# Optimization experiments

Measured on AMD Instinct MI355X. Metric: run time of the kernel, lower is better.

The kernel has to match this reference:

```python
import jax, jax.numpy as jnp
import numpy as np

N_HEADS = 8
EMBED = 640
CROSS = 768
HEAD = EMBED // N_HEADS


def setup_inputs() -> dict:
    key = jax.random.key(0)
    ks = jax.random.split(key, 10)
    s_e = 1.0 / np.sqrt(EMBED)
    s_c = 1.0 / np.sqrt(CROSS)
    return {
        "x": jax.random.normal(ks[0], (8, 4096, EMBED), jnp.float32),
        "y": jax.random.normal(ks[1], (8, 77, CROSS), jnp.float32),
        "Wq": jax.random.uniform(ks[2], (EMBED, EMBED), jnp.float32, -s_e, s_e),
        "bq": jax.random.uniform(ks[3], (EMBED,), jnp.float32, -s_e, s_e),
        "Wk": jax.random.uniform(ks[4], (CROSS, EMBED), jnp.float32, -s_c, s_c),
        "bk": jax.random.uniform(ks[5], (EMBED,), jnp.float32, -s_c, s_c),
        "Wv": jax.random.uniform(ks[6], (CROSS, EMBED), jnp.float32, -s_c, s_c),
        "bv": jax.random.uniform(ks[7], (EMBED,), jnp.float32, -s_c, s_c),
        "Wo": jax.random.uniform(ks[8], (EMBED, EMBED), jnp.float32, -s_e, s_e),
        "bo": jax.random.uniform(ks[9], (EMBED,), jnp.float32, -s_e, s_e),
    }


def reference(x, y, Wq, bq, Wk, bk, Wv, bv, Wo, bo):
    B, T, C = x.shape
    S = y.shape[1]
    # projections; split heads: [B, H, T, D]
    q = (x @ Wq + bq).reshape(B, T, N_HEADS, HEAD).transpose(0, 2, 1, 3)
    k = (y @ Wk + bk).reshape(B, S, N_HEADS, HEAD).transpose(0, 2, 1, 3)
    v = (y @ Wv + bv).reshape(B, S, N_HEADS, HEAD).transpose(0, 2, 1, 3)
    scores = jnp.einsum("bhtd,bhsd->bhts", q, k) / jnp.sqrt(jnp.float32(HEAD))
    attn = jax.nn.softmax(scores, axis=-1)
    out = jnp.einsum("bhts,bhsd->bhtd", attn, v)
    out = out.transpose(0, 2, 1, 3).reshape(B, T, C)
    return out @ Wo + bo
```

## Files before the change

### kernel.cpp

```cpp
#include <hip/hip_runtime.h>
#include <hip/hip_bf16.h>
#include <hip/hip_fp16.h>

#define EMBED 640
#define CROSS 768
#define NH 8
#define HEAD 80
#define BATCH 8
#define SEQT 4096
#define SEQS 77
#define MROWS (BATCH * SEQT)

typedef _Float16 half8 __attribute__((ext_vector_type(8)));
typedef float floatx4 __attribute__((ext_vector_type(4)));

__device__ __forceinline__ void lds_load16(const void* g, void* l) {
    __builtin_amdgcn_global_load_lds(
        (const __attribute__((address_space(1))) void*)g,
        (__attribute__((address_space(3))) void*)l, 16, 0, 0);
}

__global__ __launch_bounds__(256) void cvt_f32_f16(
    const float* __restrict__ in, _Float16* __restrict__ out)
{
    size_t i = ((size_t)blockIdx.x * 256 + threadIdx.x) * 8;
    float4 a = *(const float4*)&in[i];
    float4 b = *(const float4*)&in[i + 4];
    half8 h;
    h[0] = (_Float16)a.x; h[1] = (_Float16)a.y;
    h[2] = (_Float16)a.z; h[3] = (_Float16)a.w;
    h[4] = (_Float16)b.x; h[5] = (_Float16)b.y;
    h[6] = (_Float16)b.z; h[7] = (_Float16)b.w;
    *(half8*)&out[i] = h;
}

__global__ __launch_bounds__(256) void transpose_all(
    const float* __restrict__ Wq, const float* __restrict__ Wo,
    const float* __restrict__ Wk, const float* __restrict__ Wv,
    _Float16* __restrict__ wqt, _Float16* __restrict__ wot,
    _Float16* __restrict__ wkt, _Float16* __restrict__ wvt)
{
    __shared__ float t[32][33];
    const int z = blockIdx.z;
    const float* W;  _Float16* Wt;  int K;
    if      (z == 0) { W = Wq; Wt = wqt; K = EMBED; }
    else if (z == 1) { W = Wo; Wt = wot; K = EMBED; }
    else if (z == 2) { W = Wk; Wt = wkt; K = CROSS; }
    else             { W = Wv; Wt = wvt; K = CROSS; }
    const int N = EMBED;
    const int k0 = blockIdx.y * 32, n0 = blockIdx.x * 32;
    if (k0 >= K) return;
    for (int r = threadIdx.y; r < 32; r += 8)
        t[r][threadIdx.x] = W[(size_t)(k0 + r) * N + n0 + threadIdx.x];
    __syncthreads();
    for (int r = threadIdx.y; r < 32; r += 8)
        Wt[(size_t)(n0 + r) * K + k0 + threadIdx.x] = (_Float16)t[threadIdx.x][r];
}

__global__ __launch_bounds__(256) void cvt_y_zero(
    const float* __restrict__ y, _Float16* __restrict__ yh,
    _Float16* __restrict__ vth)
{
    const size_t i = (size_t)blockIdx.x * 256 + threadIdx.x;
    if (i < (size_t)640 * CROSS / 8) {
        const size_t e = i * 8;
        half8 h = {};
        if (e < (size_t)BATCH * SEQS * CROSS) {
            float4 a = *(const float4*)&y[e];
            float4 b = *(const float4*)&y[e + 4];
            h[0] = (_Float16)a.x; h[1] = (_Float16)a.y;
            h[2] = (_Float16)a.z; h[3] = (_Float16)a.w;
            h[4] = (_Float16)b.x; h[5] = (_Float16)b.y;
            h[6] = (_Float16)b.z; h[7] = (_Float16)b.w;
        }
        *(half8*)&yh[e] = h;
    } else {
        const size_t j = (i - (size_t)640 * CROSS / 8) * 8;
        *(half8*)&vth[j] = (half8){};
    }
}

template <bool HALF_OUT>
__global__ __launch_bounds__(256) void gemm_f16(
    const _Float16* __restrict__ A,
    const _Float16* __restrict__ Bt,
    const float* __restrict__ bias,
    void* __restrict__ Cout, int M, int N, int K, float scale)
{
    __shared__ _Float16 As[2][128 * 64];
    __shared__ _Float16 Bs[2][128 * 64];

    const int tid  = threadIdx.x;
    const int wave = tid >> 6;
    const int lane = tid & 63;
    const int quad = lane >> 4;
    const int l16  = lane & 15;

    const int l   = blockIdx.y * gridDim.x + blockIdx.x;
    const int inner = l >> 3;
    const int p   = (l & 7) + 8 * (inner / gridDim.x);
    const int nt  = inner % gridDim.x;
    const int m0 = p * 128, n0 = nt * 128;
    const int wm = (wave >> 1) * 64, wn = (wave & 1) * 64;

    const int srow = wave * 32 + (lane >> 3);
    const int sch  = ((lane & 7) ^ (lane >> 3)) * 8;
    const _Float16* gA[4];
    const _Float16* gB[4];
    #pragma unroll
    for (int q = 0; q < 4; ++q) {
        gA[q] = &A [(size_t)(m0 + srow + q * 8) * K + sch];
        gB[q] = &Bt[(size_t)(n0 + srow + q * 8) * K + sch];
    }

    const int NT = K / 64;

    auto stage = [&](int t, int bf) {
        const size_t off = (size_t)t * 64;
        #pragma unroll
        for (int q = 0; q < 4; ++q) {
            lds_load16(gA[q] + off, &As[bf][(wave * 4 + q) * 512]);
            lds_load16(gB[q] + off, &Bs[bf][(wave * 4 + q) * 512]);
        }
    };
    stage(0, 0);

    floatx4 acc[4][4] = {};

    for (int t = 0; t < NT; ++t) {
        const int bf = t & 1;
        if (t + 1 < NT) {
            stage(t + 1, bf ^ 1);
            asm volatile("s_waitcnt vmcnt(8)" ::: "memory");
        } else {
            asm volatile("s_waitcnt vmcnt(0)" ::: "memory");
        }
        __builtin_amdgcn_s_barrier();
        __builtin_amdgcn_sched_barrier(0);

        const _Float16* as = As[bf];
        const _Float16* bs = Bs[bf];
        __builtin_amdgcn_s_setprio(1);
        #pragma unroll
        for (int k = 0; k < 2; ++k) {
            half8 a[4], b[4];
            #pragma unroll
            for (int i = 0; i < 4; ++i)
                a[i] = *(const half8*)&as[(wm + i * 16 + l16) * 64 +
                                          (((k * 4 + quad) ^ (l16 & 7)) * 8)];
            #pragma unroll
            for (int j = 0; j < 4; ++j)
                b[j] = *(const half8*)&bs[(wn + j * 16 + l16) * 64 +
                                          (((k * 4 + quad) ^ (l16 & 7)) * 8)];
            #pragma unroll
            for (int i = 0; i < 4; ++i)
                #pragma unroll
                for (int j = 0; j < 4; ++j)
                    acc[i][j] = __builtin_amdgcn_mfma_f32_16x16x32_f16(
                        a[i], b[j], acc[i][j], 0, 0, 0);
        }
        __builtin_amdgcn_s_setprio(0);

        asm volatile("s_waitcnt lgkmcnt(0)" ::: "memory");
        __builtin_amdgcn_sched_barrier(0);
        __builtin_amdgcn_s_barrier();
    }

    float bcol[4];
    #pragma unroll
    for (int j = 0; j < 4; ++j) bcol[j] = bias[n0 + wn + j * 16 + l16];
    #pragma unroll
    for (int i = 0; i < 4; ++i)
        #pragma unroll
        for (int r = 0; r < 4; ++r) {
            const int m = m0 + wm + i * 16 + quad * 4 + r;
            #pragma unroll
            for (int j = 0; j < 4; ++j) {
                float v = (acc[i][j][r] + bcol[j]) * scale;
                const size_t off = (size_t)m * N + n0 + wn + j * 16 + l16;
                if (HALF_OUT) ((_Float16*)Cout)[off] = (_Float16)v;
                else          ((float*)Cout)[off] = v;
            }
        }
}

__global__ __launch_bounds__(256) void kv_gemm(
    const _Float16* __restrict__ yh,
    const _Float16* __restrict__ Wkt, const _Float16* __restrict__ Wvt,
    const float* __restrict__ bk, const float* __restrict__ bv,
    _Float16* __restrict__ kh, _Float16* __restrict__ vth)
{
    __shared__ _Float16 As[64 * 32];
    __shared__ _Float16 Bs[64 * 32];

    const int tid = threadIdx.x;
    const int wave = tid >> 6, lane = tid & 63;
    const int quad = lane >> 4, l16 = lane & 15;
    const int m0 = blockIdx.y * 64, n0 = blockIdx.x * 64;
    const bool isV = blockIdx.z != 0;
    const _Float16* Bt = isV ? Wvt : Wkt;
    const float* bias  = isV ? bv : bk;

    const int row = tid >> 2;
    const int kch = (tid & 3) * 8;

    floatx4 acc[4] = {};

    for (int k0 = 0; k0 < CROSS; k0 += 32) {
        lds_load16(&yh[(size_t)(m0 + row) * CROSS + k0 + kch], &As[wave * 512]);
        lds_load16(&Bt[(size_t)(n0 + row) * CROSS + k0 + kch], &Bs[wave * 512]);
        __syncthreads();
        half8 b = *(const half8*)&Bs[(wave * 16 + l16) * 32 + quad * 8];
        #pragma unroll
        for (int i = 0; i < 4; ++i) {
            half8 a = *(const half8*)&As[(i * 16 + l16) * 32 + quad * 8];
            acc[i] = __builtin_amdgcn_mfma_f32_16x16x32_f16(a, b, acc[i], 0, 0, 0);
        }
        __syncthreads();
    }

    const int n = n0 + wave * 16 + l16;
    const int h = n / HEAD, d = n % HEAD;
    const float bb = bias[n];
    #pragma unroll
    for (int i = 0; i < 4; ++i)
        #pragma unroll
        for (int r = 0; r < 4; ++r) {
            const int m = m0 + i * 16 + quad * 4 + r;
            if (m >= BATCH * SEQS) continue;
            const int b_ = m / SEQS, s = m % SEQS;
            const int bh = b_ * NH + h;
            const float v = acc[i][r] + bb;
            if (isV) vth[(size_t)bh * (HEAD * 80) + d * 80 + s] = (_Float16)v;
            else     kh [(size_t)bh * (SEQS * HEAD) + s * HEAD + d] = (_Float16)v;
        }
}

__global__ __launch_bounds__(256, 4) void attn_mfma(
    const _Float16* __restrict__ qh,
    const _Float16* __restrict__ kh,
    const _Float16* __restrict__ vth,
    _Float16* __restrict__ oh)
{
    constexpr int LS = 88;
    __shared__ _Float16 lds[(80 + 80 + 64) * LS + 8];
    _Float16* Ks = lds;
    _Float16* Vt = lds + 80 * LS;
    _Float16* Ps = lds + 160 * LS;

    const int tid = threadIdx.x;
    const int wave = tid >> 6, lane = tid & 63;
    const int quad = lane >> 4, l16 = lane & 15;
    const int bh = blockIdx.y;
    const int b = bh >> 3, h = bh & 7;
    const size_t row0 = (size_t)b * SEQT + (size_t)blockIdx.x * 256;
    const half8 hz = {};

    const _Float16* qp = qh + (row0 + wave * 16 + l16) * EMBED + h * HEAD;

    half8 qa0 = *(const half8*)&qp[quad * 8];
    half8 qa1 = *(const half8*)&qp[32 + quad * 8];
    half8 qa2 = (quad < 2) ? *(const half8*)&qp[64 + quad * 8] : hz;

    for (int idx = tid; idx < 80 * 11; idx += 256) {
        const int s = idx / 11, c = idx % 11;
        half8 v = hz;
        if (s < SEQS && c < 10)
            v = *(const half8*)&kh[(size_t)bh * (SEQS * HEAD) + s * HEAD + c * 8];
        *(half8*)&Ks[s * LS + c * 8] = v;
    }
    for (int idx = tid; idx < 80 * 11; idx += 256) {
        const int d = idx / 11, c = idx % 11;
        half8 v = hz;
        if (c < 10)
            v = *(const half8*)&vth[(size_t)bh * (HEAD * 80) + d * 80 + c * 8];
        *(half8*)&Vt[d * LS + c * 8] = v;
    }
    __syncthreads();

    for (int t = 0; t < 4; ++t) {
        floatx4 accs[5] = {};
        #pragma unroll
        for (int st = 0; st < 5; ++st) {
            const _Float16* kr = &Ks[(st * 16 + l16) * LS];
            half8 b0 = *(const half8*)&kr[quad * 8];
            half8 b1 = *(const half8*)&kr[32 + quad * 8];
            half8 b2 = *(const half8*)&kr[64 + quad * 8];
            accs[st] = __builtin_amdgcn_mfma_f32_16x16x32_f16(qa0, b0, accs[st], 0, 0, 0);
            accs[st] = __builtin_amdgcn_mfma_f32_16x16x32_f16(qa1, b1, accs[st], 0, 0, 0);
            accs[st] = __builtin_amdgcn_mfma_f32_16x16x32_f16(qa2, b2, accs[st], 0, 0, 0);
        }
        if (l16 >= 13) {
            accs[4][0] = -1e30f; accs[4][1] = -1e30f;
            accs[4][2] = -1e30f; accs[4][3] = -1e30f;
        }

        float recip[4];
        #pragma unroll
        for (int r = 0; r < 4; ++r) {
            float m = accs[0][r];
            #pragma unroll
            for (int st = 1; st < 5; ++st) m = fmaxf(m, accs[st][r]);
            m = fmaxf(m, __shfl_xor(m, 1));
            m = fmaxf(m, __shfl_xor(m, 2));
            m = fmaxf(m, __shfl_xor(m, 4));
            m = fmaxf(m, __shfl_xor(m, 8));
            float l = 0.f;
            const int row = wave * 16 + quad * 4 + r;
            #pragma unroll
            for (int st = 0; st < 5; ++st) {
                float e = __expf(accs[st][r] - m);
                l += e;
                Ps[row * LS + st * 16 + l16] = (_Float16)e;
            }
            l += __shfl_xor(l, 1);
            l += __shfl_xor(l, 2);
            l += __shfl_xor(l, 4);
            l += __shfl_xor(l, 8);
            recip[r] = 1.0f / l;
        }
        __syncthreads();

        half8 qn0 = hz, qn1 = hz, qn2 = hz;
        if (t < 3) {
            const _Float16* qn = qp + (size_t)(t + 1) * 64 * EMBED;
            qn0 = *(const half8*)&qn[quad * 8];
            qn1 = *(const half8*)&qn[32 + quad * 8];
            if (quad < 2) qn2 = *(const half8*)&qn[64 + quad * 8];
        }

        const _Float16* pr = &Ps[(wave * 16 + l16) * LS];
        half8 pa0 = *(const half8*)&pr[quad * 8];
        half8 pa1 = *(const half8*)&pr[32 + quad * 8];
        half8 pa2 = (quad < 2) ? *(const half8*)&pr[64 + quad * 8] : hz;
        __syncthreads();

        floatx4 acco[5] = {};
        #pragma unroll
        for (int dt = 0; dt < 5; ++dt) {
            const _Float16* vr = &Vt[(dt * 16 + l16) * LS];
            half8 b0 = *(const half8*)&vr[quad * 8];
            half8 b1 = *(const half8*)&vr[32 + quad * 8];
            half8 b2 = *(const half8*)&vr[64 + quad * 8];
            acco[dt] = __builtin_amdgcn_mfma_f32_16x16x32_f16(pa0, b0, acco[dt], 0, 0, 0);
            acco[dt] = __builtin_amdgcn_mfma_f32_16x16x32_f16(pa1, b1, acco[dt], 0, 0, 0);
            acco[dt] = __builtin_amdgcn_mfma_f32_16x16x32_f16(pa2, b2, acco[dt], 0, 0, 0);
        }

        #pragma unroll
        for (int r = 0; r < 4; ++r) {
            const size_t grow = row0 + t * 64 + wave * 16 + quad * 4 + r;
            #pragma unroll
            for (int dt = 0; dt < 5; ++dt)
                oh[grow * EMBED + h * HEAD + dt * 16 + l16] =
                    (_Float16)(acco[dt][r] * recip[r]);
        }

        qa0 = qn0; qa1 = qn1; qa2 = qn2;
    }
}

extern "C" void kernel_launch(void* const* d_in, const int* in_sizes, int n_in,
                              void* d_out, int out_size, void* d_ws, size_t ws_size,
                              hipStream_t stream)
{
    const float* x  = (const float*)d_in[0];
    const float* y  = (const float*)d_in[1];
    const float* Wq = (const float*)d_in[2];
    const float* bq = (const float*)d_in[3];
    const float* Wk = (const float*)d_in[4];
    const float* bk = (const float*)d_in[5];
    const float* Wv = (const float*)d_in[6];
    const float* bv = (const float*)d_in[7];
    const float* Wo = (const float*)d_in[8];
    const float* bo = (const float*)d_in[9];
    float* out = (float*)d_out;

    const size_t ME = (size_t)MROWS * EMBED;
    _Float16* xh  = (_Float16*)d_ws;
    _Float16* qh  = xh + ME;
    _Float16* ah  = qh + ME;
    _Float16* kh  = ah + ME;
    _Float16* vth = kh  + (size_t)BATCH * NH * SEQS * HEAD;
    _Float16* wqt = vth + (size_t)BATCH * NH * HEAD * 80;
    _Float16* wot = wqt + (size_t)EMBED * EMBED;
    _Float16* yh  = wot + (size_t)EMBED * EMBED;
    _Float16* wkt = yh  + (size_t)640 * CROSS;
    _Float16* wvt = wkt + (size_t)EMBED * CROSS;

    transpose_all<<<dim3(EMBED / 32, CROSS / 32, 4), dim3(32, 8), 0, stream>>>(
        Wq, Wo, Wk, Wv, wqt, wot, wkt, wvt);
    cvt_y_zero<<<dim3(440), 256, 0, stream>>>(y, yh, vth);
    cvt_f32_f16<<<dim3(ME / (256 * 8)), 256, 0, stream>>>(x, xh);

    gemm_f16<true><<<dim3(EMBED / 128, MROWS / 128), 256, 0, stream>>>(
        xh, wqt, bq, qh, MROWS, EMBED, EMBED, 0.11180339887498949f);
    kv_gemm<<<dim3(EMBED / 64, 640 / 64, 2), 256, 0, stream>>>(
        yh, wkt, wvt, bk, bv, kh, vth);
    attn_mfma<<<dim3(SEQT / 256, BATCH * NH), 256, 0, stream>>>(qh, kh, vth, ah);
    gemm_f16<false><<<dim3(EMBED / 128, MROWS / 128), 256, 0, stream>>>(
        ah, wot, bo, out, MROWS, EMBED, EMBED, 1.0f);
}
```

Before: 288.2 us.

## Fuse fp32-to-fp16 conversion of x into the Q projection GEMM

Removes the standalone cvt_f32_f16 pass over x and adds a dedicated gemm_q kernel. It loads fp32 x tiles into registers, converts them to fp16 and writes them into swizzled LDS, while B tiles are staged with direct global-to-LDS loads in a double-buffered pipeline. This saves a full write and re-read of the fp16 copy of x (about 42 MB of traffic) and one kernel launch. In exchange the GEMM reads twice as many bytes for A, holds more registers for the prefetched fp32 data, and relies on hand-placed waitcnt counts being right.

```diff
diff --git a/kernel.cpp b/kernel.cpp
--- a/kernel.cpp
+++ b/kernel.cpp
@@ -18,20 +18,6 @@
     __builtin_amdgcn_global_load_lds(
         (const __attribute__((address_space(1))) void*)g,
         (__attribute__((address_space(3))) void*)l, 16, 0, 0);
-}
-
-__global__ __launch_bounds__(256) void cvt_f32_f16(
-    const float* __restrict__ in, _Float16* __restrict__ out)
-{
-    size_t i = ((size_t)blockIdx.x * 256 + threadIdx.x) * 8;
-    float4 a = *(const float4*)&in[i];
-    float4 b = *(const float4*)&in[i + 4];
-    half8 h;
-    h[0] = (_Float16)a.x; h[1] = (_Float16)a.y;
-    h[2] = (_Float16)a.z; h[3] = (_Float16)a.w;
-    h[4] = (_Float16)b.x; h[5] = (_Float16)b.y;
-    h[6] = (_Float16)b.z; h[7] = (_Float16)b.w;
-    *(half8*)&out[i] = h;
 }
 
 __global__ __launch_bounds__(256) void transpose_all(
@@ -184,6 +170,148 @@
         }
 }
 
+__global__ __launch_bounds__(256) void gemm_q(
+    const float* __restrict__ x,
+    const _Float16* __restrict__ Bt,
+    const float* __restrict__ bias,
+    _Float16* __restrict__ Cout)
+{
+    constexpr int K = EMBED, N = EMBED;
+    __shared__ _Float16 As[2][128 * 64];
+    __shared__ _Float16 Bs[2][128 * 64];
+
+    const int tid  = threadIdx.x;
+    const int wave = tid >> 6;
+    const int lane = tid & 63;
+    const int quad = lane >> 4;
+    const int l16  = lane & 15;
+
+    const int l   = blockIdx.y * gridDim.x + blockIdx.x;
+    const int inner = l >> 3;
+    const int p   = (l & 7) + 8 * (inner / gridDim.x);
+    const int nt  = inner % gridDim.x;
+    const int m0 = p * 128, n0 = nt * 128;
+    const int wm = (wave >> 1) * 64, wn = (wave & 1) * 64;
+
+    const int srow = wave * 32 + (lane >> 3);
+    const int sch  = ((lane & 7) ^ (lane >> 3)) * 8;
+    const _Float16* gB[4];
+    #pragma unroll
+    for (int q = 0; q < 4; ++q)
+        gB[q] = &Bt[(size_t)(n0 + srow + q * 8) * K + sch];
+
+    const int ar = tid >> 1, ah = tid & 1;
+    const float* gA = &x[(size_t)(m0 + ar) * K + ah * 32];
+    int wslot[4];
+    #pragma unroll
+    for (int j = 0; j < 4; ++j) wslot[j] = ((ah * 4 + j) ^ (ar & 7)) * 8;
+
+    constexpr int NT = K / 64;
+
+    auto stageB = [&](int t, int bf) {
+        #pragma unroll
+        for (int q = 0; q < 4; ++q)
+            lds_load16(gB[q] + (size_t)t * 64, &Bs[bf][(wave * 4 + q) * 512]);
+    };
+    auto loadA = [&](float4 (&a)[8], int t) {
+        #pragma unroll
+        for (int j = 0; j < 8; ++j)
+            a[j] = *(const float4*)(gA + (size_t)t * 64 + j * 4);
+    };
+    auto writeA = [&](const float4 (&a)[8], int bf) {
+        #pragma unroll
+        for (int j = 0; j < 4; ++j) {
+            const float4 u = a[2 * j], v = a[2 * j + 1];
+            half8 h;
+            h[0] = (_Float16)u.x; h[1] = (_Float16)u.y;
+            h[2] = (_Float16)u.z; h[3] = (_Float16)u.w;
+            h[4] = (_Float16)v.x; h[5] = (_Float16)v.y;
+            h[6] = (_Float16)v.z; h[7] = (_Float16)v.w;
+            *(half8*)&As[bf][ar * 64 + wslot[j]] = h;
+        }
+    };
+
+    floatx4 acc[4][4] = {};
+    auto compute = [&](int bf) {
+        const _Float16* as = As[bf];
+        const _Float16* bs = Bs[bf];
+        __builtin_amdgcn_s_setprio(1);
+        #pragma unroll
+        for (int k = 0; k < 2; ++k) {
+            half8 a[4], b[4];
+            #pragma unroll
+            for (int i = 0; i < 4; ++i)
+                a[i] = *(const half8*)&as[(wm + i * 16 + l16) * 64 +
+                                          (((k * 4 + quad) ^ (l16 & 7)) * 8)];
+            #pragma unroll
+            for (int j = 0; j < 4; ++j)
+                b[j] = *(const half8*)&bs[(wn + j * 16 + l16) * 64 +
+                                          (((k * 4 + quad) ^ (l16 & 7)) * 8)];
+            #pragma unroll
+            for (int i = 0; i < 4; ++i)
+                #pragma unroll
+                for (int j = 0; j < 4; ++j)
+                    acc[i][j] = __builtin_amdgcn_mfma_f32_16x16x32_f16(
+                        a[i], b[j], acc[i][j], 0, 0, 0);
+        }
+        __builtin_amdgcn_s_setprio(0);
+    };
+
+    float4 aP[8], aQ[8];
+
+    stageB(0, 0);
+    loadA(aP, 0);
+
+    for (int t = 0; t < NT; t += 2) {
+        stageB(t + 1, 1);
+        loadA(aQ, t + 1);
+        asm volatile("s_waitcnt vmcnt(12)" ::: "memory");
+        __builtin_amdgcn_sched_barrier(0);
+        writeA(aP, 0);
+        asm volatile("s_waitcnt lgkmcnt(0)" ::: "memory");
+        __builtin_amdgcn_sched_barrier(0);
+        __builtin_amdgcn_s_barrier();
+        __builtin_amdgcn_sched_barrier(0);
+        compute(0);
+        asm volatile("s_waitcnt lgkmcnt(0)" ::: "memory");
+        __builtin_amdgcn_sched_barrier(0);
+        __builtin_amdgcn_s_barrier();
+
+        if (t + 2 < NT) {
+            stageB(t + 2, 0);
+            loadA(aP, t + 2);
+            asm volatile("s_waitcnt vmcnt(12)" ::: "memory");
+        } else {
+            asm volatile("s_waitcnt vmcnt(0)" ::: "memory");
+        }
+        __builtin_amdgcn_sched_barrier(0);
+        writeA(aQ, 1);
+        asm volatile("s_waitcnt lgkmcnt(0)" ::: "memory");
+        __builtin_amdgcn_sched_barrier(0);
+        __builtin_amdgcn_s_barrier();
+        __builtin_amdgcn_sched_barrier(0);
+        compute(1);
+        asm volatile("s_waitcnt lgkmcnt(0)" ::: "memory");
+        __builtin_amdgcn_sched_barrier(0);
+        __builtin_amdgcn_s_barrier();
+    }
+
+    const float scale = 0.11180339887498949f;
+    float bcol[4];
+    #pragma unroll
+    for (int j = 0; j < 4; ++j) bcol[j] = bias[n0 + wn + j * 16 + l16];
+    #pragma unroll
+    for (int i = 0; i < 4; ++i)
+        #pragma unroll
+        for (int r = 0; r < 4; ++r) {
+            const int m = m0 + wm + i * 16 + quad * 4 + r;
+            #pragma unroll
+            for (int j = 0; j < 4; ++j)
+                Cout[(size_t)m * N + n0 + wn + j * 16 + l16] =
+                    (_Float16)((acc[i][j][r] + bcol[j]) * scale);
+        }
+}
+
 __global__ __launch_bounds__(256) void kv_gemm(
     const _Float16* __restrict__ yh,
     const _Float16* __restrict__ Wkt, const _Float16* __restrict__ Wvt,
@@ -377,8 +505,7 @@
     float* out = (float*)d_out;
 
     const size_t ME = (size_t)MROWS * EMBED;
-    _Float16* xh  = (_Float16*)d_ws;
-    _Float16* qh  = xh + ME;
+    _Float16* qh  = (_Float16*)d_ws;
     _Float16* ah  = qh + ME;
     _Float16* kh  = ah + ME;
     _Float16* vth = kh  + (size_t)BATCH * NH * SEQS * HEAD;
@@ -391,10 +518,8 @@
     transpose_all<<<dim3(EMBED / 32, CROSS / 32, 4), dim3(32, 8), 0, stream>>>(
         Wq, Wo, Wk, Wv, wqt, wot, wkt, wvt);
     cvt_y_zero<<<dim3(440), 256, 0, stream>>>(y, yh, vth);
-    cvt_f32_f16<<<dim3(ME / (256 * 8)), 256, 0, stream>>>(x, xh);
-
-    gemm_f16<true><<<dim3(EMBED / 128, MROWS / 128), 256, 0, stream>>>(
-        xh, wqt, bq, qh, MROWS, EMBED, EMBED, 0.11180339887498949f);
+
+    gemm_q<<<dim3(EMBED / 128, MROWS / 128), 256, 0, stream>>>(x, wqt, bq, qh);
     kv_gemm<<<dim3(EMBED / 64, 640 / 64, 2), 256, 0, stream>>>(
         yh, wkt, wvt, bk, bv, kh, vth);
     attn_mfma<<<dim3(SEQT / 256, BATCH * NH), 256, 0, stream>>>(qh, kh, vth, ah);
```

Result: slower. 307.9 us (+6.8%).
